# Kernel optimization log

Hardware: AMD Instinct MI355X
Metric: run time of the kernel (lower is better)

The kernel has to match this reference:

```python
import jax, jax.numpy as jnp
import numpy as np

COUPLE_STRENGTH = 0.1
ITER_FISTA = 16
ITER_EIGENVAL = 20


def setup_inputs() -> dict:
    key = jax.random.key(0)
    k1, k2 = jax.random.split(key)
    # light field patches: (b, N, u, v, s, t, ch)
    x = jax.random.normal(k1, (8, 256, 5, 5, 4, 4, 3), dtype=jnp.float32)
    dim_signal = 5 * 5 * 4 * 4 * 3  # 1200
    dim_dict = 2 * dim_signal       # overcompleteness = 2 -> 2400
    D = jax.random.normal(k2, (dim_signal, dim_dict), dtype=jnp.float32)
    D = D / jnp.linalg.norm(D, axis=0, keepdims=True)  # UnitNorm(axis=0) constraint
    return {"x": x, "dictionary": D}


def _max_eigval(D):
    """von Mises power iteration for largest eigenvalue of D^T D."""
    v0 = jax.random.normal(jax.random.key(42), (D.shape[1],), dtype=D.dtype)
    v0 = v0 / jnp.linalg.norm(v0)

    def step(v, _):
        w = D.T @ (D @ v)
        n = jnp.linalg.norm(w)
        return w / n, n

    _, norms = jax.lax.scan(step, v0, None, length=ITER_EIGENVAL)
    return norms[-1]


def _soft_threshold(x, thr):
    return jnp.sign(x) * jnp.maximum(jnp.abs(x) - thr, 0.0)


def _sparse_code_fista(x2, D):
    """x2: (B, N, dim_signal); D: (dim_signal, dim_dict) -> codes (B, N, dim_dict)."""
    L = _max_eigval(D)            # Lipschitz constant of grad of 0.5*||Dz - x||^2
    thr = COUPLE_STRENGTH / L
    z0 = jnp.zeros(x2.shape[:-1] + (D.shape[1],), dtype=x2.dtype)
    carry0 = (z0, z0, jnp.float32(1.0))  # (z, y, t)

    def step(carry, _):
        z, y, t = carry
        recon = jnp.einsum('bnk,dk->bnd', y, D)             # (B,N,ds)
        grad = jnp.einsum('bnd,dk->bnk', recon - x2, D)     # (B,N,dd)
        z_new = _soft_threshold(y - grad / L, thr)
        t_new = 0.5 * (1.0 + jnp.sqrt(1.0 + 4.0 * t * t))
        y_new = z_new + ((t - 1.0) / t_new) * (z_new - z)   # Nesterov momentum
        return (z_new, y_new, t_new), None

    (z, _, _), _ = jax.lax.scan(step, carry0, None, length=ITER_FISTA)
    return z


def reference(x, dictionary):
    B, N, u, v, s, t, ch = x.shape
    x2 = x.reshape(B, N, u * v * s * t * ch)
    code = jax.lax.stop_gradient(_sparse_code_fista(x2, dictionary))
    recon = jnp.einsum('bnk,dk->bnd', code, dictionary)  # matmul(x, D, transpose_b=True)
    return recon.reshape(B, N, u, v, s, t, ch)
```

## Files before the change

### kernel.cpp

```cpp
#include <hip/hip_runtime.h>
#include <hip/hip_bf16.h>
#include <cmath>

#define DS 1200
#define DD 2400
#define MR 2048
#define KP 1216
#define NP1 1280
#define NG 2432
#define PPI 150

typedef __attribute__((ext_vector_type(8))) short s16x8;
typedef __attribute__((ext_vector_type(4))) float f32x4;

__device__ __forceinline__ float s2f(short s) {
    union { unsigned u; float f; } c;
    c.u = ((unsigned)(unsigned short)s) << 16;
    return c.f;
}
__device__ __forceinline__ short f2s(float f) {
    __hip_bfloat16 h = __float2bfloat16(f);
    return *reinterpret_cast<short*>(&h);
}


__device__ __forceinline__ unsigned rotl32(unsigned x, int d) {
    return (x << d) | (x >> (32 - d));
}

__device__ void threefry2x32(unsigned k0, unsigned k1, unsigned x0, unsigned x1,
                             unsigned* o0, unsigned* o1) {
    unsigned ks0 = k0, ks1 = k1, ks2 = k0 ^ k1 ^ 0x1BD11BDAu;
    const int rotA[4] = {13, 15, 26, 6};
    const int rotB[4] = {17, 29, 16, 24};
    x0 += ks0; x1 += ks1;
    #pragma unroll
    for (int r = 0; r < 4; r++) { x0 += x1; x1 = rotl32(x1, rotA[r]); x1 ^= x0; }
    x0 += ks1; x1 += ks2 + 1u;
    #pragma unroll
    for (int r = 0; r < 4; r++) { x0 += x1; x1 = rotl32(x1, rotB[r]); x1 ^= x0; }
    x0 += ks2; x1 += ks0 + 2u;
    #pragma unroll
    for (int r = 0; r < 4; r++) { x0 += x1; x1 = rotl32(x1, rotA[r]); x1 ^= x0; }
    x0 += ks0; x1 += ks1 + 3u;
    #pragma unroll
    for (int r = 0; r < 4; r++) { x0 += x1; x1 = rotl32(x1, rotB[r]); x1 ^= x0; }
    x0 += ks1; x1 += ks2 + 4u;
    #pragma unroll
    for (int r = 0; r < 4; r++) { x0 += x1; x1 = rotl32(x1, rotA[r]); x1 ^= x0; }
    x0 += ks2; x1 += ks0 + 5u;
    *o0 = x0; *o1 = x1;
}

__device__ float erfinv_f32(float x) {
    float w = -logf((1.0f - x) * (1.0f + x));
    float p;
    if (w < 5.0f) {
        w -= 2.5f;
        p = 2.81022636e-08f;
        p = fmaf(p, w, 3.43273939e-07f);
        p = fmaf(p, w, -3.5233877e-06f);
        p = fmaf(p, w, -4.39150654e-06f);
        p = fmaf(p, w, 0.00021858087f);
        p = fmaf(p, w, -0.00125372503f);
        p = fmaf(p, w, -0.00417768164f);
        p = fmaf(p, w, 0.246640727f);
        p = fmaf(p, w, 1.50140941f);
    } else {
        w = sqrtf(w) - 3.0f;
        p = -0.000200214257f;
        p = fmaf(p, w, 0.000100950558f);
        p = fmaf(p, w, 0.00134934322f);
        p = fmaf(p, w, -0.00367342844f);
        p = fmaf(p, w, 0.00573950773f);
        p = fmaf(p, w, -0.0076224613f);
        p = fmaf(p, w, 0.00943887047f);
        p = fmaf(p, w, 1.00167406f);
        p = fmaf(p, w, 2.83297682f);
    }
    return p * x;
}

__device__ float bits_to_normal(unsigned bits) {
    unsigned fb = (bits >> 9) | 0x3F800000u;
    float u01 = __uint_as_float(fb) - 1.0f;
    const float lo = -0.99999994f;
    float u = u01 * 2.0f + lo;
    u = fmaxf(lo, u);
    return 1.41421356237f * erfinv_f32(u);
}

__global__ void k_init(float* __restrict__ w0, float* __restrict__ w1,
                       float* __restrict__ part) {
    int tid = threadIdx.x;
    for (int i = tid; i < 21 * PPI; i += 256) part[i] = 0.0f;
    if (tid < 32) {
        w0[2400 + tid] = 0.0f;
        w1[2400 + tid] = 0.0f;
    }
    __shared__ float red[256];
    float local2 = 0.0f;
    for (int p = tid; p < DS; p += 256) {
        unsigned r0, r1;
        threefry2x32(0u, 42u, (unsigned)p, (unsigned)(DS + p), &r0, &r1);
        float n0 = bits_to_normal(r0);
        float n1 = bits_to_normal(r1);
        w0[p] = n0;
        w0[DS + p] = n1;
        local2 += n0 * n0 + n1 * n1;
    }
    red[tid] = local2;
    __syncthreads();
    for (int s = 128; s > 0; s >>= 1) {
        if (tid < s) red[tid] += red[tid + s];
        __syncthreads();
    }
    if (tid == 0) part[0] = red[0];
}

__global__ __launch_bounds__(1024) void k_gmv(const short* __restrict__ Grm,
                                              const float* __restrict__ win,
                                              const float* __restrict__ partin,
                                              float* __restrict__ wout,
                                              float* __restrict__ partout) {
    float s2 = 0.0f;
    for (int i = 0; i < PPI; i++) s2 += partin[i];
    float rn = 1.0f / sqrtf(s2);
    int wave = threadIdx.x >> 6, lane = threadIdx.x & 63;
    int row = blockIdx.x * 16 + wave;
    const s16x8* gh = (const s16x8*)(Grm + (size_t)row * NG);
    const float4* w4 = (const float4*)win;
    float acc = 0.0f;
    #pragma unroll
    for (int i = 0; i < 5; i++) {
        int c = lane + i * 64;
        if (c < 304) {
            s16x8 h = gh[c];
            float4 wa = w4[c * 2], wb = w4[c * 2 + 1];
            acc += s2f(h[0]) * wa.x + s2f(h[1]) * wa.y;
            acc += s2f(h[2]) * wa.z + s2f(h[3]) * wa.w;
            acc += s2f(h[4]) * wb.x + s2f(h[5]) * wb.y;
            acc += s2f(h[6]) * wb.z + s2f(h[7]) * wb.w;
        }
    }
    #pragma unroll
    for (int off = 32; off > 0; off >>= 1) acc += __shfl_xor(acc, off, 64);
    __shared__ float red[16];
    if (lane == 0) {
        float val = acc * rn;
        wout[row] = val;
        red[wave] = val * val;
    }
    __syncthreads();
    if (threadIdx.x == 0) {
        float s = 0.0f;
        #pragma unroll
        for (int i = 0; i < 16; i++) s += red[i];
        partout[blockIdx.x] = s;
    }
}

__global__ void k_fin(const float* __restrict__ part20, float* __restrict__ scal) {
    if (threadIdx.x == 0) {
        float s = 0.0f;
        for (int i = 0; i < PPI; i++) s += part20[i];
        float L = sqrtf(s);
        scal[0] = L;
        scal[1] = 1.0f / L;
        scal[2] = 0.1f / L;
    }
}

__global__ void k_makeD(const float* __restrict__ D, short* __restrict__ Dp) {
    int p = blockIdx.x * 256 + threadIdx.x;
    if (p >= NP1 * NG) return;
    int tile = p >> 10, win = p & 1023;
    int row = win >> 3, e = win & 7;
    int mt = tile / (NG >> 3), ct = tile % (NG >> 3);
    int d = mt * 128 + row, n = ct * 8 + e;
    float v = (d < DS && n < DD) ? D[(size_t)d * DD + n] : 0.0f;
    Dp[p] = f2s(v);
}

__global__ void k_makeX(const float* __restrict__ x,
                        short* __restrict__ Xhi, short* __restrict__ Xlo) {
    int p = blockIdx.x * 256 + threadIdx.x;
    if (p >= MR * KP) return;
    int tile = p >> 10, win = p & 1023;
    int row = win >> 3, e = win & 7;
    int mt = tile / (KP >> 3), ct = tile % (KP >> 3);
    int m = mt * 128 + row, k = ct * 8 + e;
    float v = (k < DS) ? x[(size_t)m * DS + k] : 0.0f;
    short h = f2s(v);
    Xhi[p] = h;
    Xlo[p] = f2s(v - s2f(h));
}

__global__ void k_makeDt(const float* __restrict__ D,
                         short* __restrict__ Dthi, short* __restrict__ Dtlo) {
    __shared__ float t[32][33];
    int bc = blockIdx.x * 32;
    int bk = blockIdx.y * 32;
    int tx = threadIdx.x & 31, ty = threadIdx.x >> 5;
    for (int i = ty; i < 32; i += 8) {
        int k = bk + i, c = bc + tx;
        t[i][tx] = (k < DS && c < DD) ? D[(size_t)k * DD + c] : 0.0f;
    }
    __syncthreads();
    for (int i = ty; i < 32; i += 8) {
        int c = bc + i, k = bk + tx;
        float v = t[tx][i];
        short h = f2s(v);
        size_t po = ((size_t)(c >> 7) * (KP >> 3) + (k >> 3)) * 1024 +
                    ((c & 127) << 3) + (k & 7);
        Dthi[po] = h;
        Dtlo[po] = f2s(v - s2f(h));
    }
}

__global__ void k_makeW(const float* __restrict__ Gf, const float* __restrict__ scal,
                        short* __restrict__ Wp) {
    int i = blockIdx.x * 256 + threadIdx.x;
    if (i >= NG * NG / 8) return;
    float invL = scal[1];
    int e0 = i * 8;
    int band = e0 / (128 * NG);
    int rem = e0 - band * (128 * NG);
    int tile = rem >> 10;
    int row = (rem & 1023) >> 3;
    int m = band * 128 + row;
    int k0 = tile * 8;
    const float4* gp = (const float4*)(Gf + (size_t)m * NG + k0);
    float4 g0 = gp[0], g1 = gp[1];
    float gv[8] = {g0.x, g0.y, g0.z, g0.w, g1.x, g1.y, g1.z, g1.w};
    s16x8 wv;
    #pragma unroll
    for (int e = 0; e < 8; e++) {
        float wf = ((k0 + e == m) ? 1.0f : 0.0f) - gv[e] * invL;
        wv[e] = f2s(wf);
    }
    ((s16x8*)Wp)[i] = wv;
}

__global__ void k_fista0(const short* __restrict__ XDL, const float* __restrict__ scal,
                         short* __restrict__ Z, short* __restrict__ Y) {
    int i = blockIdx.x * 256 + threadIdx.x;
    if (i >= MR * NG / 8) return;
    float thr = scal[2];
    s16x8 xv = ((const s16x8*)XDL)[i];
    s16x8 zs;
    #pragma unroll
    for (int k = 0; k < 8; k++) {
        float gs = s2f(xv[k]);
        float az = fabsf(gs) - thr;
        float zn = (az > 0.0f) ? copysignf(az, gs) : 0.0f;
        zs[k] = f2s(zn);
    }
    ((s16x8*)Z)[i] = zs;
    ((s16x8*)Y)[i] = zs;
}

__device__ __forceinline__ void gload16(const void* g, void* l) {
    __builtin_amdgcn_global_load_lds(
        (const __attribute__((address_space(1))) unsigned int*)g,
        (__attribute__((address_space(3))) unsigned int*)l, 16, 0, 0);
}

__global__ __launch_bounds__(256, 3) void fista_gemm(
    const short* __restrict__ Yp, const short* __restrict__ Wq,
    const short* __restrict__ XDLp, const float* __restrict__ scal, float mom,
    short* __restrict__ Ynew, short* __restrict__ Zst) {
    __shared__ __align__(16) short ldsB[2][8192];

    const int tid = threadIdx.x;
    const int w = tid >> 6, lane = tid & 63;
    const int fm = lane & 15, kg = lane >> 4;
    const int wr = w >> 1, wc = w & 1;

    const int b = blockIdx.x;
    const int sv = b >> 3;
    const int bx = sv >> 2;
    const int by = (b & 7) * 4 + (sv & 3);
    const int m0 = by * 64, n0 = bx * 128;

    f32x4 acc[2][4];
    #pragma unroll
    for (int g = 0; g < 2; ++g)
        #pragma unroll
        for (int h = 0; h < 4; ++h) acc[g][h] = f32x4{0.f, 0.f, 0.f, 0.f};

    const float thr = scal[2];

    const int band = m0 & ~127, half = (m0 >> 6) & 1;
    const short* Abase = Yp + (size_t)band * NG +
                         (half * 64 + wr * 32 + fm) * 8 + kg * 1024;
    const short* Bbase = Wq + (size_t)n0 * NG + tid * 8;

    s16x8 aA0, aA1, aA2, aA3, aB0, aB1, aB2, aB3;

#define LOADA(st, r0, r1, r2, r3)                         \
    {                                                     \
        const short* p_ = Abase + (size_t)(st) * 8192;    \
        r0 = *(const s16x8*)(p_);                         \
        r1 = *(const s16x8*)(p_ + 128);                   \
        r2 = *(const s16x8*)(p_ + 4096);                  \
        r3 = *(const s16x8*)(p_ + 4224);                  \
    }
#define STAGEB(st, buf)                                   \
    {                                                     \
        const short* q_ = Bbase + (size_t)(st) * 8192;    \
        short* bp_ = &ldsB[buf][0];                       \
        gload16(q_, bp_ + w * 512);                       \
        gload16(q_ + 2048, bp_ + 2048 + w * 512);         \
        gload16(q_ + 4096, bp_ + 4096 + w * 512);         \
        gload16(q_ + 6144, bp_ + 6144 + w * 512);         \
    }
#define COMP(buf, r0, r1, r2, r3)                                              \
    {                                                                          \
        const short* bs_ = &ldsB[buf][0];                                      \
        {                                                                      \
            const int c_ = kg;                                                 \
            s16x8 b0 = *(const s16x8*)&bs_[c_ * 1024 + (wc * 64 + 0 * 16 + fm) * 8];  \
            s16x8 b1 = *(const s16x8*)&bs_[c_ * 1024 + (wc * 64 + 1 * 16 + fm) * 8];  \
            s16x8 b2 = *(const s16x8*)&bs_[c_ * 1024 + (wc * 64 + 2 * 16 + fm) * 8];  \
            s16x8 b3 = *(const s16x8*)&bs_[c_ * 1024 + (wc * 64 + 3 * 16 + fm) * 8];  \
            acc[0][0] = __builtin_amdgcn_mfma_f32_16x16x32_bf16(r0, b0, acc[0][0], 0, 0, 0); \
            acc[0][1] = __builtin_amdgcn_mfma_f32_16x16x32_bf16(r0, b1, acc[0][1], 0, 0, 0); \
            acc[0][2] = __builtin_amdgcn_mfma_f32_16x16x32_bf16(r0, b2, acc[0][2], 0, 0, 0); \
            acc[0][3] = __builtin_amdgcn_mfma_f32_16x16x32_bf16(r0, b3, acc[0][3], 0, 0, 0); \
            acc[1][0] = __builtin_amdgcn_mfma_f32_16x16x32_bf16(r1, b0, acc[1][0], 0, 0, 0); \
            acc[1][1] = __builtin_amdgcn_mfma_f32_16x16x32_bf16(r1, b1, acc[1][1], 0, 0, 0); \
            acc[1][2] = __builtin_amdgcn_mfma_f32_16x16x32_bf16(r1, b2, acc[1][2], 0, 0, 0); \
            acc[1][3] = __builtin_amdgcn_mfma_f32_16x16x32_bf16(r1, b3, acc[1][3], 0, 0, 0); \
        }                                                                      \
        {                                                                      \
            const int c_ = 4 + kg;                                             \
            s16x8 b0 = *(const s16x8*)&bs_[c_ * 1024 + (wc * 64 + 0 * 16 + fm) * 8];  \
            s16x8 b1 = *(const s16x8*)&bs_[c_ * 1024 + (wc * 64 + 1 * 16 + fm) * 8];  \
            s16x8 b2 = *(const s16x8*)&bs_[c_ * 1024 + (wc * 64 + 2 * 16 + fm) * 8];  \
            s16x8 b3 = *(const s16x8*)&bs_[c_ * 1024 + (wc * 64 + 3 * 16 + fm) * 8];  \
            acc[0][0] = __builtin_amdgcn_mfma_f32_16x16x32_bf16(r2, b0, acc[0][0], 0, 0, 0); \
            acc[0][1] = __builtin_amdgcn_mfma_f32_16x16x32_bf16(r2, b1, acc[0][1], 0, 0, 0); \
            acc[0][2] = __builtin_amdgcn_mfma_f32_16x16x32_bf16(r2, b2, acc[0][2], 0, 0, 0); \
            acc[0][3] = __builtin_amdgcn_mfma_f32_16x16x32_bf16(r2, b3, acc[0][3], 0, 0, 0); \
            acc[1][0] = __builtin_amdgcn_mfma_f32_16x16x32_bf16(r3, b0, acc[1][0], 0, 0, 0); \
            acc[1][1] = __builtin_amdgcn_mfma_f32_16x16x32_bf16(r3, b1, acc[1][1], 0, 0, 0); \
            acc[1][2] = __builtin_amdgcn_mfma_f32_16x16x32_bf16(r3, b2, acc[1][2], 0, 0, 0); \
            acc[1][3] = __builtin_amdgcn_mfma_f32_16x16x32_bf16(r3, b3, acc[1][3], 0, 0, 0); \
        }                                                                      \
    }

    LOADA(0, aA0, aA1, aA2, aA3);
    STAGEB(0, 0);

    for (int t = 0; t < 38; t += 2) {
        __syncthreads();
        STAGEB(t + 1, 1);
        LOADA(t + 1, aB0, aB1, aB2, aB3);
        COMP(0, aA0, aA1, aA2, aA3);
        __syncthreads();
        if (t + 2 < 38) {
            STAGEB(t + 2, 0);
            LOADA(t + 2, aA0, aA1, aA2, aA3);
        }
        COMP(1, aB0, aB1, aB2, aB3);
    }

#undef LOADA
#undef STAGEB
#undef COMP

    #pragma unroll
    for (int g = 0; g < 2; ++g) {
        #pragma unroll
        for (int h = 0; h < 4; ++h) {
            #pragma unroll
            for (int j = 0; j < 4; ++j) {
                int m = m0 + wr * 32 + g * 16 + kg * 4 + j;
                int n = n0 + wc * 64 + h * 16 + fm;
                float v = acc[g][h][j];
                size_t pz = (size_t)(m & ~127) * NG + ((n >> 3) << 10) +
                            ((m & 127) << 3) + (n & 7);
                float gs = v + s2f(XDLp[pz]);
                float az = fabsf(gs) - thr;
                float zn = (az > 0.0f) ? copysignf(az, gs) : 0.0f;
                float zold = s2f(Zst[pz]);
                float yn = zn + mom * (zn - zold);
                Zst[pz] = f2s(zn);
                Ynew[pz] = f2s(yn);
            }
        }
    }
}

template <int EPI, bool SPLIT>
__global__ __launch_bounds__(256, 4) void mfma_gemm(
    const short* __restrict__ Ah, const short* __restrict__ Al, int CA,
    const short* __restrict__ Bh, const short* __restrict__ Bl, int CB,
    int K, int swz,
    const float* __restrict__ scal,
    short* __restrict__ Ynew,
    short* __restrict__ Grm,
    float* __restrict__ Out) {
    constexpr int ALO = 2048;
    constexpr int BHO = 4096;
    constexpr int BLO = 8192;
    constexpr int BUF = 12288;
    __shared__ __align__(16) short lds[2 * BUF];

    const int tid = threadIdx.x;
    const int w = tid >> 6, lane = tid & 63;
    const int fm = lane & 15, kg = lane >> 4;
    const int wr = w >> 1, wc = w & 1;

    int bx, by;
    if (swz) {
        int sv = blockIdx.x >> 3;
        bx = sv >> 2;
        by = (blockIdx.x & 7) * 4 + (sv & 3);
    } else { bx = blockIdx.x; by = blockIdx.y; }
    const int m0 = by * 64, n0 = bx * 128;

    f32x4 acc[2][4];
    #pragma unroll
    for (int g = 0; g < 2; ++g)
        #pragma unroll
        for (int h = 0; h < 4; ++h) acc[g][h] = f32x4{0.f, 0.f, 0.f, 0.f};

    float invL = 0.0f;
    if (EPI == 3) invL = scal[1];

    const int half = (m0 >> 6) & 1;
    const int nk = K / (SPLIT ? 32 : 64);

    const size_t AbS = (size_t)(m0 & ~127) * CA + w * 1024 + half * 512 + lane * 8;
    const size_t BbS = (size_t)n0 * CB + w * 512 + lane * 8;
    const size_t AbN = (size_t)(m0 & ~127) * CA + half * 512 + lane * 8;
    const size_t BbN = (size_t)n0 * CB + lane * 8;

    auto STAGE = [&](int t, int cur) {
        short* bp = &lds[cur * BUF];
        if constexpr (SPLIT) {
            const size_t kk = (size_t)t << 12;
            gload16(Ah + AbS + kk, bp + w * 512);
            gload16(Bh + BbS + kk, bp + BHO + w * 512);
            gload16(Bh + BbS + kk + 2048, bp + BHO + 2048 + w * 512);
            gload16(Al + AbS + kk, bp + ALO + w * 512);
            gload16(Bl + BbS + kk, bp + BLO + w * 512);
            gload16(Bl + BbS + kk + 2048, bp + BLO + 2048 + w * 512);
        } else {
            const size_t kk = (size_t)t << 13;
            const int cs0 = 2 * w, cs1 = 2 * w + 1;
            gload16(Ah + AbN + kk + cs0 * 1024, bp + cs0 * 512);
            gload16(Ah + AbN + kk + cs1 * 1024, bp + cs1 * 512);
            gload16(Bh + BbN + kk + cs0 * 1024,       bp + BHO + cs0 * 1024);
            gload16(Bh + BbN + kk + cs0 * 1024 + 512, bp + BHO + cs0 * 1024 + 512);
            gload16(Bh + BbN + kk + cs1 * 1024,       bp + BHO + cs1 * 1024);
            gload16(Bh + BbN + kk + cs1 * 1024 + 512, bp + BHO + cs1 * 1024 + 512);
        }
    };

    STAGE(0, 0);

    for (int t = 0; t < nk; ++t) {
        __syncthreads();
        if (t + 1 < nk) STAGE(t + 1, (t + 1) & 1);
        const short* bs = &lds[(t & 1) * BUF];

        #pragma unroll
        for (int ks = 0; ks < (SPLIT ? 1 : 2); ++ks) {
            const int c = ks * 4 + kg;
            s16x8 a[2], b[4];
            #pragma unroll
            for (int g = 0; g < 2; ++g)
                a[g] = *(const s16x8*)&bs[c * 512 + (wr * 32 + g * 16 + fm) * 8];
            #pragma unroll
            for (int h = 0; h < 4; ++h)
                b[h] = *(const s16x8*)&bs[BHO + c * 1024 + (wc * 64 + h * 16 + fm) * 8];
            if constexpr (SPLIT) {
                s16x8 a2[2], b2[4];
                #pragma unroll
                for (int g = 0; g < 2; ++g)
                    a2[g] = *(const s16x8*)&bs[ALO + c * 512 + (wr * 32 + g * 16 + fm) * 8];
                #pragma unroll
                for (int h = 0; h < 4; ++h)
                    b2[h] = *(const s16x8*)&bs[BLO + c * 1024 + (wc * 64 + h * 16 + fm) * 8];
                #pragma unroll
                for (int g = 0; g < 2; ++g)
                    #pragma unroll
                    for (int h = 0; h < 4; ++h) {
                        acc[g][h] = __builtin_amdgcn_mfma_f32_16x16x32_bf16(a[g], b[h], acc[g][h], 0, 0, 0);
                        acc[g][h] = __builtin_amdgcn_mfma_f32_16x16x32_bf16(a[g], b2[h], acc[g][h], 0, 0, 0);
                        acc[g][h] = __builtin_amdgcn_mfma_f32_16x16x32_bf16(a2[g], b[h], acc[g][h], 0, 0, 0);
                    }
            } else {
                #pragma unroll
                for (int g = 0; g < 2; ++g)
                    #pragma unroll
                    for (int h = 0; h < 4; ++h)
                        acc[g][h] = __builtin_amdgcn_mfma_f32_16x16x32_bf16(a[g], b[h], acc[g][h], 0, 0, 0);
            }
        }
    }

    #pragma unroll
    for (int g = 0; g < 2; ++g) {
        #pragma unroll
        for (int h = 0; h < 4; ++h) {
            #pragma unroll
            for (int j = 0; j < 4; ++j) {
                int m = m0 + wr * 32 + g * 16 + kg * 4 + j;
                int n = n0 + wc * 64 + h * 16 + fm;
                float v = acc[g][h][j];
                if (EPI == 0) {
                    if (n < DS) Out[(size_t)m * DS + n] = v;
                } else if (EPI == 3) {
                    size_t pz = (size_t)(m & ~127) * NG + ((n >> 3) << 10) +
                                ((m & 127) << 3) + (n & 7);
                    Ynew[pz] = f2s(v * invL);
                } else {
                    size_t o = (size_t)m * NG + n;
                    Grm[o] = f2s(v);
                    Out[o] = v;
                }
            }
        }
    }
}

extern "C" void kernel_launch(void* const* d_in, const int* in_sizes, int n_in,
                              void* d_out, int out_size, void* d_ws, size_t ws_size,
                              hipStream_t stream) {
    const float* x = (const float*)d_in[0];
    const float* D = (const float*)d_in[1];
    float* out = (float*)d_out;

    char* wsb = (char*)d_ws;
    float* w0 = (float*)wsb;
    float* w1 = w0 + 2432;
    float* part = w1 + 2432;
    float* scal = part + 3200;

    char* p = wsb + 65536;
    short* Dp   = (short*)p; p += (size_t)NP1 * NG * 2;
    short* Dthi = (short*)p; p += (size_t)NG * KP * 2;
    short* Dtlo = (short*)p; p += (size_t)NG * KP * 2;
    short* Xhi  = (short*)p; p += (size_t)MR * KP * 2;
    short* Xlo  = (short*)p; p += (size_t)MR * KP * 2;
    short* Wp   = (short*)p; p += (size_t)NG * NG * 2;
    short* Grm  = (short*)p; p += (size_t)NG * NG * 2;
    short* XDLp = (short*)p; p += (size_t)MR * NG * 2;
    short* Ya   = (short*)p; p += (size_t)MR * NG * 2;
    short* Yb   = (short*)p; p += (size_t)MR * NG * 2;
    short* Zp   = (short*)p; p += (size_t)MR * NG * 2;
    float* Gf   = (float*)Ya;

    k_makeD<<<(NP1 * NG + 255) / 256, 256, 0, stream>>>(D, Dp);
    k_makeDt<<<dim3(NG / 32, KP / 32), 256, 0, stream>>>(D, Dthi, Dtlo);
    k_makeX<<<(MR * KP + 255) / 256, 256, 0, stream>>>(x, Xhi, Xlo);

    mfma_gemm<4, true><<<dim3(NG / 128, NG / 64), 256, 0, stream>>>(
        Dthi, Dtlo, KP, Dthi, Dtlo, KP, KP, 0,
        nullptr, nullptr, Grm, Gf);

    k_init<<<1, 256, 0, stream>>>(w0, w1, part);
    for (int j = 0; j < 20; j++) {
        const float* win = (j & 1) ? w1 : w0;
        float* wout = (j & 1) ? w0 : w1;
        k_gmv<<<PPI, 1024, 0, stream>>>(Grm, win, part + j * PPI, wout,
                                        part + (j + 1) * PPI);
    }
    k_fin<<<1, 64, 0, stream>>>(part + 20 * PPI, scal);

    k_makeW<<<(NG * NG / 8 + 255) / 256, 256, 0, stream>>>(Gf, scal, Wp);

    mfma_gemm<3, true><<<dim3(608), 256, 0, stream>>>(
        Xhi, Xlo, KP, Dthi, Dtlo, KP, KP, 1,
        scal, XDLp, nullptr, nullptr);

    k_fista0<<<(MR * NG / 8 + 255) / 256, 256, 0, stream>>>(XDLp, scal, Zp, Ya);

    float t = 1.6180339887f;
    for (int i = 1; i < 16; i++) {
        float tn = 0.5f * (1.0f + sqrtf(1.0f + 4.0f * t * t));
        float mom = (t - 1.0f) / tn;
        t = tn;
        short* Yc = (i & 1) ? Ya : Yb;
        short* Yn = (i & 1) ? Yb : Ya;
        fista_gemm<<<dim3(608), 256, 0, stream>>>(
            Yc, Wp, XDLp, scal, mom, Yn, Zp);
    }

    mfma_gemm<0, false><<<dim3(320), 256, 0, stream>>>(
        Zp, nullptr, NG, Dp, nullptr, NG, NG, 1,
        nullptr, nullptr, nullptr, out);
}
```

Before: 1.028 ms.

## Triple-buffer B tiles with partial vmcnt waits and remap swizzled block order

The FISTA GEMM moves from double to triple buffering of the B tile in LDS. It prefetches two stages ahead and replaces __syncthreads with s_waitcnt vmcnt(4) plus a raw barrier, so global loads for later stages can stay in flight while the current stage computes. This raises LDS use per block, which may lower occupancy at 3 blocks per CU. Separately, the swizzle in the other GEMM kernel is changed to an XCD-aware mapping based on gridDim, meant to improve L2 locality.

```diff
diff --git a/kernel.cpp b/kernel.cpp
--- a/kernel.cpp
+++ b/kernel.cpp
@@ -270,7 +270,7 @@
     const short* __restrict__ Yp, const short* __restrict__ Wq,
     const short* __restrict__ XDLp, const float* __restrict__ scal, float mom,
     short* __restrict__ Ynew, short* __restrict__ Zst) {
-    __shared__ __align__(16) short ldsB[2][8192];
+    __shared__ __align__(16) short ldsB[3 * 8192];
 
     const int tid = threadIdx.x;
     const int w = tid >> 6, lane = tid & 63;
@@ -309,7 +309,7 @@
 #define STAGEB(st, buf)                                   \
     {                                                     \
         const short* q_ = Bbase + (size_t)(st) * 8192;    \
-        short* bp_ = &ldsB[buf][0];                       \
+        short* bp_ = &ldsB[(buf) * 8192];                 \
         gload16(q_, bp_ + w * 512);                       \
         gload16(q_ + 2048, bp_ + 2048 + w * 512);         \
         gload16(q_ + 4096, bp_ + 4096 + w * 512);         \
@@ -317,7 +317,7 @@
     }
 #define COMP(buf, r0, r1, r2, r3)                                              \
     {                                                                          \
-        const short* bs_ = &ldsB[buf][0];                                      \
+        const short* bs_ = &ldsB[(buf) * 8192];                                \
         {                                                                      \
             const int c_ = kg;                                                 \
             s16x8 b0 = *(const s16x8*)&bs_[c_ * 1024 + (wc * 64 + 0 * 16 + fm) * 8];  \
@@ -352,18 +352,34 @@
 
     LOADA(0, aA0, aA1, aA2, aA3);
     STAGEB(0, 0);
-
+    STAGEB(1, 1);
+
+    int rb = 0;
     for (int t = 0; t < 38; t += 2) {
-        __syncthreads();
-        STAGEB(t + 1, 1);
+        asm volatile("s_waitcnt vmcnt(4)" ::: "memory");
+        __builtin_amdgcn_s_barrier();
+        asm volatile("" ::: "memory");
         LOADA(t + 1, aB0, aB1, aB2, aB3);
-        COMP(0, aA0, aA1, aA2, aA3);
-        __syncthreads();
-        if (t + 2 < 38) {
-            STAGEB(t + 2, 0);
-            LOADA(t + 2, aA0, aA1, aA2, aA3);
+        {
+            int sb = rb + 2; if (sb >= 3) sb -= 3;
+            if (t + 2 < 38) STAGEB(t + 2, sb);
         }
-        COMP(1, aB0, aB1, aB2, aB3);
+        COMP(rb, aA0, aA1, aA2, aA3);
+        rb = (rb == 2) ? 0 : rb + 1;
+
+        if (t + 1 < 37)
+            asm volatile("s_waitcnt vmcnt(4)" ::: "memory");
+        else
+            asm volatile("s_waitcnt vmcnt(0)" ::: "memory");
+        __builtin_amdgcn_s_barrier();
+        asm volatile("" ::: "memory");
+        if (t + 2 < 38) LOADA(t + 2, aA0, aA1, aA2, aA3);
+        {
+            int sb = rb + 2; if (sb >= 3) sb -= 3;
+            if (t + 3 < 38) STAGEB(t + 3, sb);
+        }
+        COMP(rb, aB0, aB1, aB2, aB3);
+        rb = (rb == 2) ? 0 : rb + 1;
     }
 
 #undef LOADA
@@ -415,9 +431,9 @@
 
     int bx, by;
     if (swz) {
-        int sv = blockIdx.x >> 3;
-        bx = sv >> 2;
-        by = (blockIdx.x & 7) * 4 + (sv & 3);
+        int q = gridDim.x >> 3;
+        int s = (blockIdx.x & 7) * q + (blockIdx.x >> 3);
+        by = s & 31; bx = s >> 5;
     } else { bx = blockIdx.x; by = blockIdx.y; }
     const int m0 = by * 64, n0 = bx * 128;
 
```

After: 980.1 us. -4.6%, faster.
